# Kernel optimization log

Measured on AMD Instinct MI355X. Metric: run time of the kernel, lower is better.

## Reference

```python
import jax, jax.numpy as jnp
import numpy as np

D_STATE = 512


def _compute_ssm_matrices(S, K_raw, log_gamma, d_state):
    # K = K_raw / (sigma_max(K_raw).clamp(1e-5) + 0.002)  -- hard contraction
    sigma = jnp.linalg.norm(K_raw, ord=2)  # largest singular value
    sigma = jnp.maximum(sigma, 1e-5)
    K = K_raw / (sigma + 0.002)
    K11 = K[:d_state, :d_state]
    K12 = K[:d_state, d_state:]
    K21 = K[d_state:, :d_state]
    K22 = K[d_state:, d_state:]
    gamma = jnp.exp(log_gamma)
    Sinv = jnp.linalg.inv(S)
    A = Sinv @ K11 @ S
    B = gamma * (Sinv @ K12)
    C = K21 @ S
    D = gamma * K22
    return A, B, C, D


def setup_inputs() -> dict:
    key = jax.random.key(0)
    k1, k2, k3 = jax.random.split(key, 3)
    B_sz, T, H, N, P = 16, 4096, 512, 512, 512
    u = jax.random.normal(k1, (B_sz, T, H), dtype=jnp.float32)
    state = jnp.zeros((B_sz, N), dtype=jnp.float32)
    # S initialized as I + 0.01*randn (matches init_orthogonal_spectrum)
    S = jnp.eye(N, dtype=jnp.float32) + 0.01 * jax.random.normal(k2, (N, N), dtype=jnp.float32)
    K_raw = jax.random.normal(k3, (N + P, N + H), dtype=jnp.float32)
    log_gamma = jnp.zeros((), dtype=jnp.float32)  # gamma = 1.0
    return {"u": u, "state": state, "S": S, "K_raw": K_raw, "log_gamma": log_gamma}


def reference(u, state, S, K_raw, log_gamma):
    # u: [B,T,H], state: [B,N]
    A, Bm, C, D = _compute_ssm_matrices(S, K_raw, log_gamma, D_STATE)
    AT, BT, CT, DT = A.T, Bm.T, C.T, D.T

    def step(x, u_t):
        x_new = x @ AT + u_t @ BT  # [B,N]
        return x_new, x_new

    u_tbh = jnp.swapaxes(u, 0, 1)  # [T,B,H]
    _, xs = jax.lax.scan(step, state, u_tbh)  # xs: [T,B,N] = x_1..x_T
    states = jnp.concatenate([state[:, None, :], jnp.swapaxes(xs, 0, 1)], axis=1)  # [B,T+1,N]
    pre_states = states[:, :-1, :]  # x_0..x_{T-1}
    output = pre_states @ CT + u @ DT  # [B,T,d_output]
    return output, states
```

## Files before the change

### kernel.cpp

```cpp
#include <hip/hip_runtime.h>


typedef unsigned short u16;
typedef __bf16 bf16x8 __attribute__((ext_vector_type(8)));
typedef u16    u16x8  __attribute__((ext_vector_type(8)));
typedef float  f32x4  __attribute__((ext_vector_type(4)));

static_assert(sizeof(long) == 8, "need 64-bit long");

__device__ inline u16 f2bf(float f) {
    union { float f; unsigned u; } x; x.f = f;
    unsigned r = x.u + 0x7FFFu + ((x.u >> 16) & 1u);
    return (u16)(r >> 16);
}

__device__ inline bf16x8 cvt8(float4 v0, float4 v1) {
    bf16x8 a;
    a[0] = (__bf16)v0.x; a[1] = (__bf16)v0.y; a[2] = (__bf16)v0.z; a[3] = (__bf16)v0.w;
    a[4] = (__bf16)v1.x; a[5] = (__bf16)v1.y; a[6] = (__bf16)v1.z; a[7] = (__bf16)v1.w;
    return a;
}

__device__ inline void gl2lds16(const void* g, void* l) {
    auto gp = reinterpret_cast<const __attribute__((address_space(1))) char*>(
        (unsigned long long)g);
    auto lp = reinterpret_cast<__attribute__((address_space(3))) char*>(
        (unsigned)(unsigned long long)l);
    __builtin_amdgcn_global_load_lds(gp, lp, 16, 0, 0);
}

__device__ inline void wait_vmcnt(int n) {
    switch (n) {
        case 0:  asm volatile("s_waitcnt vmcnt(0)"  ::: "memory"); break;
        case 6:  asm volatile("s_waitcnt vmcnt(6)"  ::: "memory"); break;
        case 8:  asm volatile("s_waitcnt vmcnt(8)"  ::: "memory"); break;
        case 12: asm volatile("s_waitcnt vmcnt(12)" ::: "memory"); break;
        default: asm volatile("s_waitcnt vmcnt(0)"  ::: "memory"); break;
    }
}

struct SArgs {
    const float* A1; long a1BS, a1RS; int a1Shift; unsigned a1Mask; int shiftA;
    int predLow; unsigned predMask;
    const float* A2; long a2BS, a2RS; int a2Shift; unsigned a2Mask;
    const u16* B1; const u16* B2;
    int K1c, Kc;
    const float* initP; long iBS, iRS; int iShift; unsigned iMask; float beta;
    float* Out; long oBS, oRS; int oShift; unsigned oMask;
    int sMode;
};

template<int MF>
__global__ __launch_bounds__(512, 2) void gemm_staged(SArgs g) {
    __shared__ char bstg[2][32768];
    const int tid = threadIdx.x, lane = tid & 63, wv = tid >> 6;
    const int kg = lane >> 4, l15 = lane & 15;
    const int rgw = wv >> 2, cg = wv & 3;
    const long row0 = (long)blockIdx.x * (32 * MF) + rgw * (16 * MF);
    const int cb = cg * 128;
    constexpr int LA = 2 * MF;

    int Kc = g.Kc;
    const u16* B1 = g.B1;
    const u16* B2 = g.B2;
    float* Out = g.Out;
    if (g.sMode) {
        int s = blockIdx.z + 1;
        Kc = g.K1c + 16 * s;
        B1 = g.B1 + (long)(s - 1) * 262144;
        B2 = g.B2 + (long)(4 - s) * 262144;
        Out = g.Out + (long)s * 512;
    }
    const int K1c = g.K1c;

    const float* ap1[MF]; const float* ap2[MF]; bool pr[MF];
#pragma unroll
    for (int mf = 0; mf < MF; ++mf) {
        unsigned r = (unsigned)(row0 + mf * 16 + l15);
        pr[mf] = (g.predLow == 0) || ((r & g.predMask) >= (unsigned)g.predLow);
        long ra = (long)r - g.shiftA; if (ra < 0) ra = 0;
        ap1[mf] = g.A1 + ((ra >> g.a1Shift) * g.a1BS) + ((ra & (long)g.a1Mask) * g.a1RS) + kg * 8;
        ap2[mf] = nullptr;
        if (g.A2)
            ap2[mf] = g.A2 + (((long)(r >> g.a2Shift)) * g.a2BS) + ((long)(r & g.a2Mask) * g.a2RS) + kg * 8;
    }

    f32x4 acc[MF][8];
    if (g.initP) {
#pragma unroll
        for (int mf = 0; mf < MF; ++mf)
#pragma unroll
            for (int q = 0; q < 4; ++q) {
                unsigned r = (unsigned)(row0 + mf * 16 + kg * 4 + q);
                const float* ip = g.initP + ((long)(r >> g.iShift)) * g.iBS
                                + ((long)(r & g.iMask)) * g.iRS + cb + l15;
#pragma unroll
                for (int nf = 0; nf < 8; ++nf)
                    acc[mf][nf][q] = g.beta * ip[nf * 16];
            }
    } else {
#pragma unroll
        for (int mf = 0; mf < MF; ++mf)
#pragma unroll
            for (int nf = 0; nf < 8; ++nf)
                acc[mf][nf] = (f32x4){0.f, 0.f, 0.f, 0.f};
    }

    auto stage = [&](int c) {
        const char* src = (const char*)((c < K1c) ? (B1 + (long)c * 16384)
                                                  : (B2 + (long)(c - K1c) * 16384));
        char* dst = bstg[c & 1];
        const int wo = wv << 12;
#pragma unroll
        for (int i = 0; i < 4; ++i)
            gl2lds16(src + wo + (i << 10) + (lane << 4), dst + wo + (i << 10));
    };

    auto loadA = [&](int c, float4* v0, float4* v1) {
        if (c < K1c) {
#pragma unroll
            for (int mf = 0; mf < MF; ++mf) {
                v0[mf] = *(const float4*)(ap1[mf]);
                v1[mf] = *(const float4*)(ap1[mf] + 4);
                ap1[mf] += 32;
            }
        } else {
#pragma unroll
            for (int mf = 0; mf < MF; ++mf) {
                v0[mf] = *(const float4*)(ap2[mf]);
                v1[mf] = *(const float4*)(ap2[mf] + 4);
                ap2[mf] += 32;
            }
        }
    };

    auto body = [&](int c, float4* v0, float4* v1, int buf, int wn) {
        bf16x8 af[MF];
        bool mk = (c < K1c);
#pragma unroll
        for (int mf = 0; mf < MF; ++mf) {
            bf16x8 a = cvt8(v0[mf], v1[mf]);
            if (mk && !pr[mf]) { u16x8 z = {0,0,0,0,0,0,0,0}; a = __builtin_bit_cast(bf16x8, z); }
            af[mf] = a;
        }
        if (c + 2 < Kc) loadA(c + 2, v0, v1);

        wait_vmcnt(wn);
        __builtin_amdgcn_s_barrier();

        const char* bb = bstg[buf] + kg * 8192 + (cb + l15) * 16;
#pragma unroll
        for (int nf = 0; nf < 8; ++nf) {
            u16x8 br = *(const u16x8*)(bb + nf * 256);
            bf16x8 bv = __builtin_bit_cast(bf16x8, br);
#pragma unroll
            for (int mf = 0; mf < MF; ++mf)
                acc[mf][nf] = __builtin_amdgcn_mfma_f32_16x16x32_bf16(af[mf], bv, acc[mf][nf], 0, 0, 0);
        }

        asm volatile("s_waitcnt lgkmcnt(0)" ::: "memory");
        __builtin_amdgcn_s_barrier();
        if (c + 2 < Kc) stage(c + 2);
    };

    stage(0); stage(1);
    float4 a0v0[MF], a0v1[MF], a1v0[MF], a1v1[MF];
    loadA(0, a0v0, a0v1);
    loadA(1, a1v0, a1v1);

    for (int c = 0; c + 4 <= Kc; c += 2) {
        body(c,     a0v0, a0v1, 0, 2 * LA + 4);
        body(c + 1, a1v0, a1v1, 1, 2 * LA + 4);
    }
    body(Kc - 2, a0v0, a0v1, 0, LA + 4);
    body(Kc - 1, a1v0, a1v1, 1, 0);

#pragma unroll
    for (int mf = 0; mf < MF; ++mf)
#pragma unroll
        for (int q = 0; q < 4; ++q) {
            unsigned r = (unsigned)(row0 + mf * 16 + kg * 4 + q);
            float* op = Out + ((long)(r >> g.oShift)) * g.oBS
                      + ((long)(r & g.oMask)) * g.oRS + cb + l15;
#pragma unroll
            for (int nf = 0; nf < 8; ++nf) op[nf * 16] = acc[mf][nf][q];
        }
}

struct GemmArgs {
    const float* A1; long a1RS; int shiftA;
    const u16*   Bp; long ldbN, colOff;
    const float* initP; long iRS; float beta;
    float* Out; long oRS;
    int Kit; int predLow;
    float* sumsq;
    const float* scalePtr; float cScale;
    u16* OutP; long opLd;
};

__global__ __launch_bounds__(64) void gemm_bf16(GemmArgs g) {
    const int lane = threadIdx.x & 63;
    const int kg   = lane >> 4;
    const int l15  = lane & 15;
    const unsigned row0 = blockIdx.x * 16;
    const long cb = (long)blockIdx.y * 128;

    unsigned rA = row0 + l15;
    bool pr = (g.predLow == 0) || (rA >= (unsigned)g.predLow);
    long ra = (long)rA - g.shiftA; if (ra < 0) ra = 0;
    const float* ap = g.A1 + ra * g.a1RS + kg * 8;

    f32x4 acc[8];
#pragma unroll
    for (int nf = 0; nf < 8; ++nf) acc[nf] = (f32x4){0.f, 0.f, 0.f, 0.f};

    if (g.initP) {
#pragma unroll
        for (int q = 0; q < 4; ++q) {
            unsigned r = row0 + kg * 4 + q;
            const float* ip = g.initP + (long)r * g.iRS + cb + l15;
#pragma unroll
            for (int nf = 0; nf < 8; ++nf) acc[nf][q] = g.beta * ip[nf * 16];
        }
    }

    const u16* bp = g.Bp + ((long)kg * g.ldbN + g.colOff + cb + l15) * 8;
    const long bstep = g.ldbN * 32;

    for (int kk = 0; kk < g.Kit; ++kk) {
        float4 v0 = *(const float4*)(ap);
        float4 v1 = *(const float4*)(ap + 4);
        ap += 32;
        bf16x8 a = cvt8(v0, v1);
        if (!pr) { u16x8 z = {0,0,0,0,0,0,0,0}; a = __builtin_bit_cast(bf16x8, z); }
#pragma unroll
        for (int nf = 0; nf < 8; ++nf) {
            u16x8 braw = *(const u16x8*)(bp + (long)nf * 128);
            bf16x8 bb = __builtin_bit_cast(bf16x8, braw);
            acc[nf] = __builtin_amdgcn_mfma_f32_16x16x32_bf16(a, bb, acc[nf], 0, 0, 0);
        }
        bp += bstep;
    }

    float sc = g.cScale;
    if (g.scalePtr) sc *= 1.0f / g.scalePtr[0];
    float ss = 0.f;
#pragma unroll
    for (int q = 0; q < 4; ++q) {
        unsigned r = row0 + kg * 4 + q;
        float* op = g.Out + (long)r * g.oRS + cb + l15;
#pragma unroll
        for (int nf = 0; nf < 8; ++nf) {
            float v = sc * acc[nf][q];
            op[nf * 16] = v;
            ss += v * v;
            if (g.OutP) {
                long col = cb + l15 + nf * 16;
                g.OutP[((long)(r >> 3) * g.opLd + col) * 8 + (r & 7)] = f2bf(v);
            }
        }
    }
    if (g.sumsq) {
#pragma unroll
        for (int off = 32; off; off >>= 1) ss += __shfl_down(ss, off);
        if (lane == 0) atomicAdd(g.sumsq, ss);
    }
}

__global__ __launch_bounds__(256) void gemm_f32_512(const float* A, const float* B,
                                                    const float* I, float* O,
                                                    float alpha, float beta) {
    __shared__ float As[16][68];
    __shared__ float Bs[16][68];
    const int tx = threadIdx.x & 15, ty = threadIdx.x >> 4;
    const int bm = blockIdx.x * 64, bn = blockIdx.y * 64;
    float acc[4][4] = {};
    for (int k0 = 0; k0 < 512; k0 += 16) {
        for (int t = threadIdx.x; t < 1024; t += 256) {
            int r = t >> 4, c = t & 15;
            As[c][r] = A[(long)(bm + r) * 512 + k0 + c];
            int r2 = t >> 6, c2 = t & 63;
            Bs[r2][c2] = B[(long)(k0 + r2) * 512 + bn + c2];
        }
        __syncthreads();
#pragma unroll
        for (int k = 0; k < 16; ++k)
#pragma unroll
            for (int i = 0; i < 4; ++i)
#pragma unroll
                for (int j = 0; j < 4; ++j)
                    acc[i][j] += As[k][ty * 4 + i] * Bs[k][tx * 4 + j];
        __syncthreads();
    }
#pragma unroll
    for (int i = 0; i < 4; ++i)
#pragma unroll
        for (int j = 0; j < 4; ++j) {
            long o = (long)(bm + ty * 4 + i) * 512 + bn + tx * 4 + j;
            float v = alpha * acc[i][j];
            if (I) v += beta * I[o];
            O[o] = v;
        }
}

__global__ __launch_bounds__(256) void k_cast_panel(const float* src, long srcLd, long R, long C,
                                                    u16* panel, long pLd) {
    long total = R * C;
    for (long idx = (long)blockIdx.x * 256 + threadIdx.x; idx < total; idx += (long)gridDim.x * 256) {
        long k = idx / C, n = idx % C;
        panel[((k >> 3) * pLd + n) * 8 + (k & 7)] = f2bf(src[k * srcLd + n]);
    }
}

__global__ __launch_bounds__(256) void k_transpose_cast(const float* src, long srcLd, long R, long C,
                                                        u16* panel, long pLd, float* dstFT,
                                                        const float* slots, int sIdx) {
    float scale = (sIdx >= 0) ? slots[sIdx] : 1.0f;
    long total = R * C;
    for (long idx = (long)blockIdx.x * 256 + threadIdx.x; idx < total; idx += (long)gridDim.x * 256) {
        long i = idx / C, j = idx % C;
        float v = src[i * srcLd + j] * scale;
        if (panel) panel[((j >> 3) * pLd + i) * 8 + (j & 7)] = f2bf(v);
        if (dstFT) dstFT[j * R + i] = v;
    }
}

struct T4Args {
    const float* src0; const float* src1; const float* src2; const float* src3;
    long ld0, ld1, ld2, ld3;
    u16 *p0, *p1, *p2, *p3;
    float *f0, *f1, *f2, *f3;
    int s0, s1, s2, s3;
    const float* slots;
};
__global__ __launch_bounds__(256) void k_transpose4(T4Args t) {
    int m = blockIdx.y;
    const float* src; long ld; u16* panel; float* dstFT; int sIdx;
    if (m == 0) { src = t.src0; ld = t.ld0; panel = t.p0; dstFT = t.f0; sIdx = t.s0; }
    else if (m == 1) { src = t.src1; ld = t.ld1; panel = t.p1; dstFT = t.f1; sIdx = t.s1; }
    else if (m == 2) { src = t.src2; ld = t.ld2; panel = t.p2; dstFT = t.f2; sIdx = t.s2; }
    else { src = t.src3; ld = t.ld3; panel = t.p3; dstFT = t.f3; sIdx = t.s3; }
    float scale = (sIdx >= 0) ? t.slots[sIdx] : 1.0f;
    for (long idx = (long)blockIdx.x * 256 + threadIdx.x; idx < 262144; idx += (long)gridDim.x * 256) {
        long i = idx >> 9, j = idx & 511;
        float v = src[i * ld + j] * scale;
        panel[((j >> 3) * 512 + i) * 8 + (j & 7)] = f2bf(v);
        if (dstFT) dstFT[j * 512 + i] = v;
    }
}

__global__ __launch_bounds__(256) void k_sx1(const float* S, u16* Sp, float* Xf, u16* Xp) {
    for (long idx = (long)blockIdx.x * 256 + threadIdx.x; idx < 262144; idx += (long)gridDim.x * 256) {
        int i = (int)(idx >> 9), j = (int)(idx & 511);
        float sv = S[idx];
        Sp[(((long)(i >> 3)) * 512 + j) * 8 + (i & 7)] = f2bf(sv);
        float v = ((i == j) ? 2.0f : 0.0f) - sv;
        Xf[idx] = v;
        Xp[(((long)(i >> 3)) * 512 + j) * 8 + (i & 7)] = f2bf(v);
    }
}

__global__ void k_fin(float* slots, const float* lg) {
    float lnacc = 0.f, w = 1.f;
    for (int i = 0; i <= 8; ++i) {
        lnacc += w * 0.5f * logf(fmaxf(slots[i], 1e-30f));
        w *= 0.5f;
    }
    float sigma = fmaxf(expf(0.5f * lnacc), 1e-5f);
    float s = sigma + 0.002f;
    slots[32] = 1.0f / s;
    slots[33] = expf(lg[0]) / s;
}

__global__ __launch_bounds__(256) void k_state0(float* states, const float* state) {
    int i = blockIdx.x * 256 + threadIdx.x;
    if (i < 8192) {
        int b = i >> 9, n = i & 511;
        states[(long)b * 2097664 + n] = state[i];
    }
}

extern "C" void kernel_launch(void* const* d_in, const int* in_sizes, int n_in,
                              void* d_out, int out_size, void* d_ws, size_t ws_size,
                              hipStream_t stream) {
    (void)in_sizes; (void)n_in; (void)out_size; (void)ws_size;

    const float* u     = (const float*)d_in[0];
    const float* state = (const float*)d_in[1];
    const float* S     = (const float*)d_in[2];
    const float* K     = (const float*)d_in[3];
    const float* lg    = (const float*)d_in[4];

    float* out    = (float*)d_out;
    float* states = out + 33554432L;
    float* Zb     = out;

    char* w = (char*)d_ws;
    auto alloc = [&](size_t n) { void* p = w; w += (n + 255) & ~(size_t)255; return p; };
    float* slots = (float*)alloc(256);
    u16* Qall = (u16*)alloc(4L * 262144 * 2);
    u16* W4p  = (u16*)alloc(4L * 262144 * 2);
    u16* Q8p  = (u16*)alloc(262144L * 2);
    u16* Q16p = (u16*)alloc(262144L * 2);
    u16* CDT  = (u16*)alloc(2L * 262144 * 2);
    float* Qf   = (float*)alloc(4L * 262144 * 4);
    float* W4f  = (float*)alloc(4L * 262144 * 4);
    float* Q8f  = (float*)alloc(262144L * 4);
    float* Q16f = (float*)alloc(262144L * 4);
    float* Za   = (float*)w;
    float* KTf = (float*)alloc(1024L * 1024 * 4);
    u16*   Kp  = (u16*)  alloc(1024L * 1024 * 2);
    float* Mf  = (float*)alloc(1024L * 1024 * 4);
    u16*   Mp  = (u16*)  alloc(1024L * 1024 * 2);
    float* Mf2 = (float*)alloc(1024L * 1024 * 4);
    u16*   Mp2 = (u16*)  alloc(1024L * 1024 * 2);
    u16*   Sp  = (u16*)  alloc(512L * 512 * 2);
    float* Xaf = (float*)alloc(512L * 512 * 4);
    u16*   Xap = (u16*)  alloc(512L * 512 * 2);
    float* Xbf = (float*)alloc(512L * 512 * 4);
    u16*   Xbp = (u16*)  alloc(512L * 512 * 2);
    float* Pf  = (float*)alloc(512L * 512 * 4);
    u16*   Pp  = (u16*)  alloc(512L * 512 * 2);
    float* Xs  = (float*)alloc(512L * 512 * 4);
    float* T1f = (float*)alloc(512L * 512 * 4);
    u16*   T1p = (u16*)  alloc(512L * 512 * 2);
    float* Af  = (float*)alloc(512L * 512 * 4);
    float* Bmf = (float*)alloc(512L * 512 * 4);
    float* Cmf = (float*)alloc(512L * 512 * 4);

    auto mkargs = [&]() { GemmArgs a = {}; a.beta = 1.f; a.cScale = 1.f; return a; };
    auto launch_gemm = [&](int M, int N, const GemmArgs& a) {
        dim3 gr(M / 16, N / 128);
        gemm_bf16<<<gr, 64, 0, stream>>>(a);
    };

    hipMemsetAsync(slots, 0, 256, stream);

    k_transpose_cast<<<4096, 256, 0, stream>>>(K, 1024, 1024, 1024, nullptr, 0, KTf, nullptr, -1);
    k_cast_panel<<<4096, 256, 0, stream>>>(K, 1024, 1024, 1024, Kp, 1024);
    {   GemmArgs a = mkargs();
        a.A1 = KTf; a.a1RS = 1024;
        a.Bp = Kp; a.ldbN = 1024;
        a.Out = Mf; a.oRS = 1024; a.OutP = Mp; a.opLd = 1024;
        a.Kit = 32; a.sumsq = slots + 0;
        launch_gemm(1024, 1024, a);
    }
    {   float* Fs[2] = {Mf, Mf2};
        u16*   Ps[2] = {Mp, Mp2};
        for (int i = 1; i <= 8; ++i) {
            GemmArgs a = mkargs();
            a.A1 = Fs[(i + 1) & 1]; a.a1RS = 1024;
            a.Bp = Ps[(i + 1) & 1]; a.ldbN = 1024;
            a.Out = Fs[i & 1]; a.oRS = 1024; a.OutP = Ps[i & 1]; a.opLd = 1024;
            a.Kit = 32; a.sumsq = slots + i; a.scalePtr = slots + (i - 1);
            launch_gemm(1024, 1024, a);
        }
    }
    k_fin<<<1, 1, 0, stream>>>(slots, lg);

    k_sx1<<<1024, 256, 0, stream>>>(S, Sp, Xaf, Xap);
    float* curF = Xaf; u16* curP = Xap; float* nxtF = Xbf; u16* nxtP = Xbp;
    for (int it = 0; it < 3; ++it) {
        GemmArgs a = mkargs();
        a.A1 = S; a.a1RS = 512;
        a.Bp = curP; a.ldbN = 512;
        a.Out = Pf; a.oRS = 512; a.OutP = Pp; a.opLd = 512; a.cScale = -1.f;
        a.Kit = 16;
        launch_gemm(512, 512, a);
        GemmArgs b = mkargs();
        b.A1 = curF; b.a1RS = 512;
        b.Bp = Pp; b.ldbN = 512;
        b.initP = curF; b.iRS = 512; b.beta = 2.f;
        b.Out = nxtF; b.oRS = 512; b.OutP = nxtP; b.opLd = 512;
        b.Kit = 16;
        launch_gemm(512, 512, b);
        float* tf = curF; curF = nxtF; nxtF = tf;
        u16*   tp = curP; curP = nxtP; nxtP = tp;
    }
    gemm_f32_512<<<dim3(8, 8), 256, 0, stream>>>(S, curF, nullptr, Pf, 1.f, 0.f);
    gemm_f32_512<<<dim3(8, 8), 256, 0, stream>>>(curF, Pf, curF, Xs, -1.f, 2.f);

    {   GemmArgs a = mkargs();
        a.A1 = K; a.a1RS = 1024; a.Bp = Sp; a.ldbN = 512;
        a.Out = T1f; a.oRS = 512; a.OutP = T1p; a.opLd = 512; a.Kit = 16;
        launch_gemm(512, 512, a);
    }
    {   GemmArgs a = mkargs();
        a.A1 = Xs; a.a1RS = 512; a.Bp = T1p; a.ldbN = 512;
        a.Out = Af; a.oRS = 512; a.Kit = 16;
        launch_gemm(512, 512, a);
    }
    {   GemmArgs a = mkargs();
        a.A1 = Xs; a.a1RS = 512; a.Bp = Kp; a.ldbN = 1024; a.colOff = 512;
        a.Out = Bmf; a.oRS = 512; a.Kit = 16;
        launch_gemm(512, 512, a);
    }
    {   GemmArgs a = mkargs();
        a.A1 = K + 512L * 1024; a.a1RS = 1024; a.Bp = Sp; a.ldbN = 512;
        a.Out = Cmf; a.oRS = 512; a.Kit = 16;
        launch_gemm(512, 512, a);
    }
    {   T4Args t = {};
        t.src0 = Af;  t.ld0 = 512;  t.p0 = Qall;            t.f0 = Qf;            t.s0 = 32;
        t.src1 = Bmf; t.ld1 = 512;  t.p1 = W4p + 3*262144;  t.f1 = W4f + 3*262144; t.s1 = 33;
        t.src2 = Cmf; t.ld2 = 512;  t.p2 = CDT;             t.f2 = nullptr;       t.s2 = 32;
        t.src3 = K + 512L*1024 + 512; t.ld3 = 1024; t.p3 = CDT + 262144; t.f3 = nullptr; t.s3 = 33;
        t.slots = slots;
        k_transpose4<<<dim3(512, 4), 256, 0, stream>>>(t);
    }
    {   GemmArgs a = mkargs();
        a.A1 = Qf; a.a1RS = 512; a.Bp = Qall; a.ldbN = 512;
        a.Out = Qf + 262144; a.oRS = 512; a.OutP = Qall + 262144; a.opLd = 512; a.Kit = 16;
        launch_gemm(512, 512, a);
        a.A1 = Qf; a.Bp = Qall + 262144;
        a.Out = Qf + 2 * 262144; a.OutP = Qall + 2 * 262144;
        launch_gemm(1024, 512, a);
        a.A1 = Qf + 3 * 262144; a.Bp = Qall + 3 * 262144;
        a.Out = Q8f; a.OutP = Q8p;
        launch_gemm(512, 512, a);
        a.A1 = Q8f; a.Bp = Q8p;
        a.Out = Q16f; a.OutP = Q16p;
        launch_gemm(512, 512, a);
    }
    {   GemmArgs a = mkargs();
        a.A1 = W4f + 3 * 262144; a.a1RS = 512; a.Bp = Qall; a.ldbN = 512;
        a.Out = W4f + 2 * 262144; a.oRS = 512; a.OutP = W4p + 2 * 262144; a.opLd = 512; a.Kit = 16;
        launch_gemm(512, 512, a);
        a.A1 = W4f + 2 * 262144; a.Bp = Qall + 262144;
        a.Out = W4f; a.OutP = W4p;
        launch_gemm(1024, 512, a);
    }

    {   SArgs a = {};
        a.A1 = u; a.a1BS = 2097152; a.a1RS = 2048; a.a1Shift = 10; a.a1Mask = 1023;
        a.predMask = 1023;
        a.B1 = W4p; a.B2 = W4p; a.K1c = 64; a.Kc = 64;
        a.beta = 1.f;
        a.Out = Za; a.oBS = 0; a.oRS = 512; a.oShift = 14; a.oMask = 16383;
        gemm_staged<1><<<dim3(512, 1, 1), 512, 0, stream>>>(a);
    }
    {   GemmArgs f = mkargs();
        f.A1 = state; f.a1RS = 512;
        f.Bp = Qall + 3 * 262144; f.ldbN = 512;
        f.initP = Za; f.iRS = 524288; f.beta = 1.f;
        f.Out = Za; f.oRS = 524288; f.Kit = 16;
        launch_gemm(16, 512, f);
    }
    k_state0<<<32, 256, 0, stream>>>(states, state);

    auto ks = [&](const float* src, float* dst, int d, const u16* gen) {
        SArgs a = {};
        a.A1 = src; a.a1BS = 0; a.a1RS = 512; a.a1Shift = 14; a.a1Mask = 16383;
        a.shiftA = d; a.predLow = d; a.predMask = 1023;
        a.B1 = gen; a.B2 = gen; a.K1c = 16; a.Kc = 16;
        a.initP = src; a.iBS = 0; a.iRS = 512; a.iShift = 14; a.iMask = 16383; a.beta = 1.f;
        a.Out = dst; a.oBS = 0; a.oRS = 512; a.oShift = 14; a.oMask = 16383;
        gemm_staged<1><<<dim3(512, 1, 1), 512, 0, stream>>>(a);
    };
    ks(Za, Zb, 1, Qall + 3 * 262144);
    ks(Zb, Za, 2, Q8p);
    {
        SArgs a = {};
        a.A1 = Za; a.a1BS = 0; a.a1RS = 512; a.a1Shift = 14; a.a1Mask = 16383;
        a.shiftA = 4; a.predLow = 4; a.predMask = 1023;
        a.B1 = Q16p; a.B2 = Q16p; a.K1c = 16; a.Kc = 16;
        a.initP = Za; a.iBS = 0; a.iRS = 512; a.iShift = 14; a.iMask = 16383; a.beta = 1.f;
        a.Out = states + 2048; a.oBS = 2097664; a.oRS = 2048; a.oShift = 10; a.oMask = 1023;
        gemm_staged<1><<<dim3(512, 1, 1), 512, 0, stream>>>(a);
    }

    {   SArgs a = {};
        a.A1 = states; a.a1BS = 2097664; a.a1RS = 2048; a.a1Shift = 10; a.a1Mask = 1023;
        a.predMask = 1023;
        a.A2 = u; a.a2BS = 2097152; a.a2RS = 2048; a.a2Shift = 10; a.a2Mask = 1023;
        a.B1 = Qall; a.B2 = W4p; a.K1c = 16; a.Kc = 0;
        a.beta = 1.f;
        a.Out = states; a.oBS = 2097664; a.oRS = 2048; a.oShift = 10; a.oMask = 1023;
        a.sMode = 1;
        gemm_staged<2><<<dim3(256, 1, 3), 512, 0, stream>>>(a);
    }

    {   SArgs a = {};
        a.A1 = states; a.a1BS = 2097664; a.a1RS = 512; a.a1Shift = 12; a.a1Mask = 4095;
        a.predMask = 4095;
        a.A2 = u; a.a2BS = 2097152; a.a2RS = 512; a.a2Shift = 12; a.a2Mask = 4095;
        a.B1 = CDT; a.B2 = CDT + 262144; a.K1c = 16; a.Kc = 32;
        a.beta = 1.f;
        a.Out = out; a.oBS = 2097152; a.oRS = 512; a.oShift = 12; a.oMask = 4095;
        gemm_staged<2><<<dim3(1024, 1, 1), 512, 0, stream>>>(a);
    }
}
```

Measured before the change: 1.207 ms.

## Add LDS-staged square GEMM for power iteration, merge K·S GEMMs, interleave stage grid

Adds a dedicated gemm_sq kernel for the 1024x1024 power-iteration squarings. It stages B panels into LDS with double buffering and shares each panel across two waves, and it fuses the scale, sum-of-squares and bf16 repack into its epilogue. It merges the two K·S GEMMs for A and C into one launch over 1024 rows by placing Cmf right after T1f. The staged sMode kernel now spreads its three segments across blockIdx.x instead of z, which changes block scheduling order. The new kernel trades generality for better reuse, but uses small 128-thread blocks, which may underfill the device.

```diff
diff --git a/kernel.cpp b/kernel.cpp
--- a/kernel.cpp
+++ b/kernel.cpp
@@ -56,21 +56,23 @@
     const int tid = threadIdx.x, lane = tid & 63, wv = tid >> 6;
     const int kg = lane >> 4, l15 = lane & 15;
     const int rgw = wv >> 2, cg = wv & 3;
-    const long row0 = (long)blockIdx.x * (32 * MF) + rgw * (16 * MF);
     const int cb = cg * 128;
     constexpr int LA = 2 * MF;
 
+    long bx = blockIdx.x;
     int Kc = g.Kc;
     const u16* B1 = g.B1;
     const u16* B2 = g.B2;
     float* Out = g.Out;
     if (g.sMode) {
-        int s = blockIdx.z + 1;
+        int s = (int)(bx % 3) + 1;
+        bx /= 3;
         Kc = g.K1c + 16 * s;
         B1 = g.B1 + (long)(s - 1) * 262144;
         B2 = g.B2 + (long)(4 - s) * 262144;
         Out = g.Out + (long)s * 512;
     }
+    const long row0 = bx * (32 * MF) + rgw * (16 * MF);
     const int K1c = g.K1c;
 
     const float* ap1[MF]; const float* ap2[MF]; bool pr[MF];
@@ -185,6 +187,87 @@
 #pragma unroll
             for (int nf = 0; nf < 8; ++nf) op[nf * 16] = acc[mf][nf][q];
         }
+}
+
+struct SqArgs {
+    const float* A;
+    const u16* Bp;
+    float* Out;
+    u16* OutP;
+    float* sumsq;
+    const float* scalePtr;
+};
+
+__global__ __launch_bounds__(128) void gemm_sq(SqArgs g) {
+    __shared__ char bstg[2][16384];
+    const int tid = threadIdx.x, lane = tid & 63, wv = tid >> 6;
+    const int kg = lane >> 4, l15 = lane & 15;
+    const int row0 = blockIdx.x * 16;
+    const int colB = blockIdx.y * 256;
+    const int cb = wv * 128;
+
+    const float* ap = g.A + (long)(row0 + l15) * 1024 + kg * 8;
+
+    f32x4 acc[8];
+#pragma unroll
+    for (int nf = 0; nf < 8; ++nf) acc[nf] = (f32x4){0.f, 0.f, 0.f, 0.f};
+
+    auto stage = [&](int c) {
+        char* dst = bstg[c & 1];
+#pragma unroll
+        for (int kq2 = 0; kq2 < 2; ++kq2) {
+            int kq = wv * 2 + kq2;
+            const char* src = (const char*)(g.Bp + ((long)(c * 4 + kq) * 1024 + colB) * 8);
+            char* d = dst + kq * 4096;
+#pragma unroll
+            for (int i = 0; i < 4; ++i)
+                gl2lds16(src + i * 1024 + lane * 16, d + i * 1024);
+        }
+    };
+
+    stage(0); stage(1);
+    float4 pv0 = *(const float4*)ap;
+    float4 pv1 = *(const float4*)(ap + 4);
+    ap += 32;
+    __syncthreads();
+
+    for (int c = 0; c < 32; ++c) {
+        bf16x8 a = cvt8(pv0, pv1);
+        if (c + 1 < 32) {
+            pv0 = *(const float4*)ap;
+            pv1 = *(const float4*)(ap + 4);
+            ap += 32;
+        }
+        const char* bb = bstg[c & 1] + kg * 4096 + (cb + l15) * 16;
+#pragma unroll
+        for (int nf = 0; nf < 8; ++nf) {
+            u16x8 br = *(const u16x8*)(bb + nf * 256);
+            acc[nf] = __builtin_amdgcn_mfma_f32_16x16x32_bf16(
+                a, __builtin_bit_cast(bf16x8, br), acc[nf], 0, 0, 0);
+        }
+        __syncthreads();
+        if (c + 2 < 32) stage(c + 2);
+    }
+
+    float sc = 1.0f;
+    if (g.scalePtr) sc = 1.0f / g.scalePtr[0];
+    float ss = 0.f;
+#pragma unroll
+    for (int q = 0; q < 4; ++q) {
+        int r = row0 + kg * 4 + q;
+        float* op = g.Out + (long)r * 1024 + colB + cb + l15;
+#pragma unroll
+        for (int nf = 0; nf < 8; ++nf) {
+            float v = sc * acc[nf][q];
+            op[nf * 16] = v;
+            ss += v * v;
+            int col = colB + cb + l15 + nf * 16;
+            g.OutP[((long)(r >> 3) * 1024 + col) * 8 + (r & 7)] = f2bf(v);
+        }
+    }
+#pragma unroll
+    for (int off = 32; off; off >>= 1) ss += __shfl_down(ss, off);
+    if (lane == 0) atomicAdd(g.sumsq, ss);
 }
 
 struct GemmArgs {
@@ -422,11 +505,11 @@
     float* Pf  = (float*)alloc(512L * 512 * 4);
     u16*   Pp  = (u16*)  alloc(512L * 512 * 2);
     float* Xs  = (float*)alloc(512L * 512 * 4);
-    float* T1f = (float*)alloc(512L * 512 * 4);
-    u16*   T1p = (u16*)  alloc(512L * 512 * 2);
+    float* T1f = (float*)alloc(1024L * 512 * 4);
+    u16*   T1p = (u16*)  alloc(1024L * 512 * 2);
+    float* Cmf = T1f + 262144;
     float* Af  = (float*)alloc(512L * 512 * 4);
     float* Bmf = (float*)alloc(512L * 512 * 4);
-    float* Cmf = (float*)alloc(512L * 512 * 4);
 
     auto mkargs = [&]() { GemmArgs a = {}; a.beta = 1.f; a.cScale = 1.f; return a; };
     auto launch_gemm = [&](int M, int N, const GemmArgs& a) {
@@ -438,22 +521,15 @@
 
     k_transpose_cast<<<4096, 256, 0, stream>>>(K, 1024, 1024, 1024, nullptr, 0, KTf, nullptr, -1);
     k_cast_panel<<<4096, 256, 0, stream>>>(K, 1024, 1024, 1024, Kp, 1024);
-    {   GemmArgs a = mkargs();
-        a.A1 = KTf; a.a1RS = 1024;
-        a.Bp = Kp; a.ldbN = 1024;
-        a.Out = Mf; a.oRS = 1024; a.OutP = Mp; a.opLd = 1024;
-        a.Kit = 32; a.sumsq = slots + 0;
-        launch_gemm(1024, 1024, a);
+    {   SqArgs q = {KTf, Kp, Mf, Mp, slots + 0, nullptr};
+        gemm_sq<<<dim3(64, 4), 128, 0, stream>>>(q);
     }
     {   float* Fs[2] = {Mf, Mf2};
         u16*   Ps[2] = {Mp, Mp2};
         for (int i = 1; i <= 8; ++i) {
-            GemmArgs a = mkargs();
-            a.A1 = Fs[(i + 1) & 1]; a.a1RS = 1024;
-            a.Bp = Ps[(i + 1) & 1]; a.ldbN = 1024;
-            a.Out = Fs[i & 1]; a.oRS = 1024; a.OutP = Ps[i & 1]; a.opLd = 1024;
-            a.Kit = 32; a.sumsq = slots + i; a.scalePtr = slots + (i - 1);
-            launch_gemm(1024, 1024, a);
+            SqArgs q = {Fs[(i + 1) & 1], Ps[(i + 1) & 1],
+                        Fs[i & 1], Ps[i & 1], slots + i, slots + (i - 1)};
+            gemm_sq<<<dim3(64, 4), 128, 0, stream>>>(q);
         }
     }
     k_fin<<<1, 1, 0, stream>>>(slots, lg);
@@ -483,7 +559,7 @@
     {   GemmArgs a = mkargs();
         a.A1 = K; a.a1RS = 1024; a.Bp = Sp; a.ldbN = 512;
         a.Out = T1f; a.oRS = 512; a.OutP = T1p; a.opLd = 512; a.Kit = 16;
-        launch_gemm(512, 512, a);
+        launch_gemm(1024, 512, a);
     }
     {   GemmArgs a = mkargs();
         a.A1 = Xs; a.a1RS = 512; a.Bp = T1p; a.ldbN = 512;
@@ -495,15 +571,10 @@
         a.Out = Bmf; a.oRS = 512; a.Kit = 16;
         launch_gemm(512, 512, a);
     }
-    {   GemmArgs a = mkargs();
-        a.A1 = K + 512L * 1024; a.a1RS = 1024; a.Bp = Sp; a.ldbN = 512;
-        a.Out = Cmf; a.oRS = 512; a.Kit = 16;
-        launch_gemm(512, 512, a);
-    }
     {   T4Args t = {};
-        t.src0 = Af;  t.ld0 = 512;  t.p0 = Qall;            t.f0 = Qf;            t.s0 = 32;
+        t.src0 = Af;  t.ld0 = 512;  t.p0 = Qall;            t.f0 = Qf;             t.s0 = 32;
         t.src1 = Bmf; t.ld1 = 512;  t.p1 = W4p + 3*262144;  t.f1 = W4f + 3*262144; t.s1 = 33;
-        t.src2 = Cmf; t.ld2 = 512;  t.p2 = CDT;             t.f2 = nullptr;       t.s2 = 32;
+        t.src2 = Cmf; t.ld2 = 512;  t.p2 = CDT;             t.f2 = nullptr;        t.s2 = 32;
         t.src3 = K + 512L*1024 + 512; t.ld3 = 1024; t.p3 = CDT + 262144; t.f3 = nullptr; t.s3 = 33;
         t.slots = slots;
         k_transpose4<<<dim3(512, 4), 256, 0, stream>>>(t);
@@ -577,7 +648,7 @@
         a.beta = 1.f;
         a.Out = states; a.oBS = 2097664; a.oRS = 2048; a.oShift = 10; a.oMask = 1023;
         a.sMode = 1;
-        gemm_staged<2><<<dim3(256, 1, 3), 512, 0, stream>>>(a);
+        gemm_staged<2><<<dim3(768, 1, 1), 512, 0, stream>>>(a);
     }
 
     {   SArgs a = {};
```

Result: slower. 1.274 ms (+5.5%).
